# Optimization experiments

Hardware: AMD Instinct MI355X
Metric: run time of the kernel (lower is better)

The kernel has to match this reference:

```python
import jax, jax.numpy as jnp
import numpy as np

NUM_CLASSES = 81
OUTPUT_SIZE = 19
NMS_THRESH = 0.45
TOP_K = 400          # pre-NMS candidates per class == max_output_size of tf NMS
KEEP_TOP_K = 200
CONF_THRESH = 0.01
MASK_CONF_THRESH = 0.6
B = 8
P = 24564


def setup_inputs() -> dict:
    key = jax.random.key(0)
    k1, k2, k3, k4 = jax.random.split(key, 4)
    # structured x = [loc | conf | priorbox | variances] so the decode math is realistic
    loc = 0.1 * jax.random.normal(k1, (B, P, 4), dtype=jnp.float32)
    conf = jax.random.uniform(k2, (B, P, NUM_CLASSES), dtype=jnp.float32)
    cxcy = jax.random.uniform(k3, (P, 2), minval=0.05, maxval=0.95)
    wh = jax.random.uniform(k4, (P, 2), minval=0.05, maxval=0.3)
    pmin = jnp.clip(cxcy - 0.5 * wh, 0.0, 1.0)
    pmax = jnp.clip(cxcy + 0.5 * wh, 0.0, 1.0)
    priors = jnp.broadcast_to(jnp.concatenate([pmin, pmax], -1), (B, P, 4)).astype(jnp.float32)
    variances = jnp.full((B, P, 4), 0.1, dtype=jnp.float32)
    x = jnp.concatenate([loc, conf, priors, variances], -1)
    return {"x": x}


def decode_boxes(loc, prior, var):
    pw = prior[..., 2] - prior[..., 0]
    ph = prior[..., 3] - prior[..., 1]
    pcx = 0.5 * (prior[..., 2] + prior[..., 0])
    pcy = 0.5 * (prior[..., 3] + prior[..., 1])
    cx = loc[..., 0] * pw * var[..., 0] + pcx
    cy = loc[..., 1] * pw * var[..., 1] + pcy  # uses prior_width, faithful to original code
    w = jnp.exp(loc[..., 2] * var[..., 2]) * pw
    h = jnp.exp(loc[..., 3] * var[..., 3]) * ph
    box = jnp.stack([cx - 0.5 * w, cy - 0.5 * h, cx + 0.5 * w, cy + 0.5 * h], -1)
    return jnp.clip(box, 0.0, 1.0)


def iou_matrix(b):  # [N,4] xyxy -> [N,N]
    area = (b[:, 2] - b[:, 0]) * (b[:, 3] - b[:, 1])
    ix1 = jnp.maximum(b[:, None, 0], b[None, :, 0])
    iy1 = jnp.maximum(b[:, None, 1], b[None, :, 1])
    ix2 = jnp.minimum(b[:, None, 2], b[None, :, 2])
    iy2 = jnp.minimum(b[:, None, 3], b[None, :, 3])
    inter = jnp.maximum(ix2 - ix1, 0.0) * jnp.maximum(iy2 - iy1, 0.0)
    union = area[:, None] + area[None, :] - inter
    return jnp.where(union > 0.0, inter / union, 0.0)


def greedy_nms(iou, valid):  # candidates already sorted desc by score
    n = valid.shape[0]
    def body(kept, i):
        sup = jnp.any(kept & (iou[i] > NMS_THRESH))
        return kept.at[i].set(valid[i] & ~sup), None
    kept, _ = jax.lax.scan(body, jnp.zeros(n, dtype=bool), jnp.arange(n))
    return kept


def _forward(x):
    b = x.shape[0]
    loc = x[..., :4]
    conf = x[..., 4:4 + NUM_CLASSES]
    prior = x[..., -8:-4]
    var = x[..., -4:]
    boxes = decode_boxes(loc, prior, var)                        # [B,P,4]
    cls_conf = jnp.swapaxes(conf[..., 1:], 1, 2)                 # [B,C-1,P] (skip background class 0)
    masked = jnp.where(cls_conf > CONF_THRESH, cls_conf, -1.0)
    scores, idx = jax.lax.top_k(masked, TOP_K)                   # [B,C-1,K]
    cand = jnp.take_along_axis(boxes[:, None], idx[..., None], axis=2)  # [B,C-1,K,4]
    valid = scores > CONF_THRESH
    iou = jax.vmap(jax.vmap(iou_matrix))(cand)                   # [B,C-1,K,K]
    kept = jax.vmap(jax.vmap(greedy_nms))(iou, valid)            # [B,C-1,K]
    labels = jnp.broadcast_to(jnp.arange(1, NUM_CLASSES)[None, :, None], scores.shape)
    det_scores = jnp.where(kept, scores, -1.0).reshape(b, -1)
    det_boxes = cand.reshape(b, -1, 4)
    det_labels = labels.reshape(b, -1)
    order = jnp.argsort(-det_scores, axis=1)[:, :KEEP_TOP_K]     # sort desc by conf, keep_top_k=200
    top_s = jnp.take_along_axis(det_scores, order, 1)            # [B,200]
    top_b = jnp.take_along_axis(det_boxes, order[..., None], 1)  # [B,200,4]
    top_l = jnp.take_along_axis(det_labels, order, 1)            # [B,200]

    def rasterize(s, bx, lb):
        vld = s >= MASK_CONF_THRESH
        co = jnp.round(bx * OUTPUT_SIZE).astype(jnp.int32)       # [K,4] x1,y1,x2,y2
        g = jnp.arange(OUTPUT_SIZE)
        cover = ((g[None, :, None] >= co[:, 1, None, None]) & (g[None, :, None] < co[:, 3, None, None]) &
                 (g[None, None, :] >= co[:, 0, None, None]) & (g[None, None, :] < co[:, 2, None, None]) &
                 vld[:, None, None])                             # [K,S,S]
        chan = lb - 1                                            # label-1 channel, as in original
        kidx = jnp.arange(KEEP_TOP_K)
        def per_channel(c):
            cov = cover & (chan == c)[:, None, None]
            win = jnp.max(jnp.where(cov, kidx[:, None, None], -1), axis=0)  # [S,S]
            return jnp.where(win >= 0, s[jnp.clip(win, 0)], 0.0)
        return jnp.transpose(jax.vmap(per_channel)(jnp.arange(NUM_CLASSES)), (1, 2, 0))

    return jax.vmap(rasterize)(top_s, top_b, top_l)              # [B,S,S,C]


def reference(x):
    return _forward(x)
```

## Files before the change

kernel.cpp:

```cpp
#include <hip/hip_runtime.h>

#define NB 8
#define NP 24564
#define NCLS 80
#define TOPK 400
#define KEEPK 200
#define OUTS 19
#define NCELL (OUTS * OUTS)
#define DETN (NCLS * TOPK)
#define CKS 32008
#define ROWS 64
#define CHUNKS ((NP + ROWS - 1) / ROWS)
#define CAP 1024
#define T0 0.972f
#define NT 512
#define LCAP 16
#define CSTR 16
#define WTASK 2704
#define SKW(i) ((unsigned)(i) + ((unsigned)(i) >> 5))
#define SELN (TOPK + (TOPK >> 5) + 4)

__device__ __forceinline__ unsigned f2ord(float f) {
    unsigned u = __float_as_uint(f);
    return (u & 0x80000000u) ? ~u : (u | 0x80000000u);
}
__device__ __forceinline__ float ord2f(unsigned k) {
    unsigned u = (k & 0x80000000u) ? (k & 0x7fffffffu) : ~k;
    return __uint_as_float(u);
}
__device__ __forceinline__ unsigned bin16(unsigned key) {
    int b = (int)(key >> 16) - 0xBC00;
    b = b < 0 ? 0 : (b > 1023 ? 1023 : b);
    return (unsigned)b;
}

__device__ __forceinline__ unsigned long long shfl_xor_u64(unsigned long long v, int mask) {
    unsigned lo = (unsigned)__shfl_xor((int)(unsigned)v, mask);
    unsigned hi = (unsigned)__shfl_xor((int)(v >> 32), mask);
    return ((unsigned long long)hi << 32) | lo;
}

__device__ __forceinline__ void regsort1024(unsigned long long& a0, unsigned long long& a1,
                                            unsigned long long* sc, unsigned t) {
    const unsigned e0 = 2u * t;
#pragma unroll
    for (unsigned k = 2; k <= 1024; k <<= 1) {
#pragma unroll
        for (unsigned j = k >> 1; j >= 128; j >>= 1) {
            sc[e0] = a0; sc[e0 + 1] = a1;
            __syncthreads();
            unsigned p0 = e0 ^ j;
            unsigned long long b0 = sc[p0], b1 = sc[p0 + 1];
            bool km = ((e0 & k) == 0u) ^ ((e0 & j) != 0u);
            a0 = km ? (a0 > b0 ? a0 : b0) : (a0 < b0 ? a0 : b0);
            a1 = km ? (a1 > b1 ? a1 : b1) : (a1 < b1 ? a1 : b1);
            __syncthreads();
        }
#pragma unroll
        for (unsigned j = ((k >> 1) < 64u ? (k >> 1) : 64u); j >= 2; j >>= 1) {
            unsigned long long b0 = shfl_xor_u64(a0, (int)(j >> 1));
            unsigned long long b1 = shfl_xor_u64(a1, (int)(j >> 1));
            bool km = ((e0 & k) == 0u) ^ ((e0 & j) != 0u);
            a0 = km ? (a0 > b0 ? a0 : b0) : (a0 < b0 ? a0 : b0);
            a1 = km ? (a1 > b1 ? a1 : b1) : (a1 < b1 ? a1 : b1);
        }
        {
            bool dir = ((e0 & k) == 0u);
            unsigned long long mx = a0 > a1 ? a0 : a1;
            unsigned long long mn = a0 > a1 ? a1 : a0;
            a0 = dir ? mx : mn;
            a1 = dir ? mn : mx;
        }
    }
}

__device__ __forceinline__ void bitonic_desc(unsigned long long* cand, unsigned S, int tid) {
    for (unsigned k = 2; k <= S; k <<= 1)
        for (unsigned j = k >> 1; j; j >>= 1) {
            for (unsigned i = tid; i < S; i += NT) {
                unsigned l = i ^ j;
                if (l > i) {
                    unsigned long long a = cand[i], bq = cand[l];
                    bool sw = ((i & k) == 0) ? (a < bq) : (a > bq);
                    if (sw) { cand[i] = bq; cand[l] = a; }
                }
            }
            __syncthreads();
        }
}

__global__ __launch_bounds__(256) void kZ(unsigned* __restrict__ ccnt,
                                          unsigned* __restrict__ gflag,
                                          unsigned* __restrict__ kcnt) {
    int t = blockIdx.x * 256 + threadIdx.x;
    for (int i = t; i < NB * NCLS * CSTR; i += gridDim.x * 256) ccnt[i] = 0u;
    if (t < NB * NCLS) gflag[t] = 0u;
    if (t < NB * 16) kcnt[t] = 0u;
}

__global__ __launch_bounds__(NT) void kA(const float* __restrict__ x,
                                         float4* __restrict__ boxes,
                                         unsigned long long* __restrict__ pcand,
                                         unsigned* __restrict__ ccnt,
                                         unsigned* __restrict__ gflag) {
    __shared__ float tile[ROWS * 93];
    __shared__ unsigned long long list[NCLS * LCAP];
    __shared__ unsigned lcnt[NCLS];
    __shared__ unsigned lbase[NCLS];

    int blk = blockIdx.x;
    int b = blk / CHUNKS, chunk = blk % CHUNKS;
    int p0 = chunk * ROWS;
    int nrows = NP - p0; if (nrows > ROWS) nrows = ROWS;
    const float* src = x + (size_t)(b * NP + p0) * 93;
    int total4 = (nrows * 93) >> 2;
    const float4* s4 = (const float4*)src;
    float4* t4 = (float4*)tile;
    for (int e = threadIdx.x; e < total4; e += NT) t4[e] = s4[e];
    __syncthreads();

    int row = threadIdx.x & 63;
    int lane = row;
    int cg = threadIdx.x >> 6;
    unsigned p = (unsigned)(p0 + row);
    bool rowOk = row < nrows;
    for (int c = cg; c < NCLS; c += (NT / 64)) {
        float v = rowOk ? tile[row * 93 + 5 + c] : -1.0f;
        bool pred = v > T0;
        unsigned long long bal = __ballot(pred);
        if (pred) {
            unsigned rank = (unsigned)__popcll(bal & ((1ull << lane) - 1ull));
            if (rank < LCAP)
                list[c * LCAP + rank] =
                    ((unsigned long long)f2ord(v) << 32) | (unsigned)(~p);
        }
        if (lane == 0) lcnt[c] = (unsigned)__popcll(bal);
    }

    if (threadIdx.x < nrows) {
        const float* r = tile + threadIdx.x * 93;
        float l0 = r[0], l1 = r[1], l2 = r[2], l3 = r[3];
        float px1 = r[85], py1 = r[86], px2 = r[87], py2 = r[88];
        float v0 = r[89], v1 = r[90], v2 = r[91], v3 = r[92];
        float pw = px2 - px1, ph = py2 - py1;
        float pcx = 0.5f * (px2 + px1), pcy = 0.5f * (py2 + py1);
        float cx = l0 * pw * v0 + pcx;
        float cy = l1 * pw * v1 + pcy;
        float w = expf(l2 * v2) * pw;
        float h = expf(l3 * v3) * ph;
        float x1 = fminf(fmaxf(cx - 0.5f * w, 0.f), 1.f);
        float y1 = fminf(fmaxf(cy - 0.5f * h, 0.f), 1.f);
        float x2 = fminf(fmaxf(cx + 0.5f * w, 0.f), 1.f);
        float y2 = fminf(fmaxf(cy + 0.5f * h, 0.f), 1.f);
        boxes[(size_t)b * NP + p0 + threadIdx.x] = make_float4(x1, y1, x2, y2);
    }
    __syncthreads();

    if (threadIdx.x < NCLS) {
        unsigned n = lcnt[threadIdx.x];
        unsigned wr = (n > LCAP) ? LCAP : n;
        lbase[threadIdx.x] =
            wr ? atomicAdd(&ccnt[(b * NCLS + threadIdx.x) * CSTR], wr) : 0u;
        lcnt[threadIdx.x] = wr;
        if (n > LCAP) gflag[b * NCLS + threadIdx.x] = 1u;
    }
    __syncthreads();

    for (int idx = threadIdx.x; idx < NCLS * LCAP; idx += NT) {
        int c = idx >> 4, i = idx & (LCAP - 1);
        if ((unsigned)i < lcnt[c]) {
            unsigned pos = lbase[c] + (unsigned)i;
            if (pos < CAP)
                pcand[((size_t)(b * NCLS + c) << 10) + pos] = list[idx];
        }
    }
}

__device__ void select_strided(const float* __restrict__ src, unsigned needed,
                               unsigned long long* cand,
                               unsigned* hist, unsigned* aux, unsigned* scal,
                               int tid) {
    for (int i = tid; i < 1024; i += NT) hist[i] = 0u;
    if (tid == 0) { scal[0] = 0u; scal[1] = 0u; scal[2] = 0u; scal[3] = 0u; }
    __syncthreads();
    for (int p = tid; p < NP; p += NT) {
        float v = src[(size_t)p * 93];
        float m = (v > 0.01f) ? v : -1.0f;
        atomicAdd(&hist[bin16(f2ord(m))], 1u);
    }
    __syncthreads();
    unsigned h0 = 0, h1 = 0, h2 = 0, h3 = 0;
    if (tid < 256) {
        h0 = hist[4 * tid]; h1 = hist[4 * tid + 1];
        h2 = hist[4 * tid + 2]; h3 = hist[4 * tid + 3];
        aux[tid] = h0 + h1 + h2 + h3;
    }
    __syncthreads();
    for (int d = 1; d < 256; d <<= 1) {
        unsigned v = 0u;
        if (tid < 256 && tid + d < 256) v = aux[tid + d];
        __syncthreads();
        if (tid < 256) aux[tid] += v;
        __syncthreads();
    }
    if (tid < 256) {
        unsigned above = (tid < 255) ? aux[tid + 1] : 0u;
        unsigned s3 = above + h3, s2 = s3 + h2, s1 = s2 + h1, s0 = s1 + h0;
        if (s0 >= needed && s1 < needed) { scal[0] = 4 * tid;     scal[1] = s1;    scal[2] = s0; }
        if (s1 >= needed && s2 < needed) { scal[0] = 4 * tid + 1; scal[1] = s2;    scal[2] = s1; }
        if (s2 >= needed && s3 < needed) { scal[0] = 4 * tid + 2; scal[1] = s3;    scal[2] = s2; }
        if (s3 >= needed && above < needed) { scal[0] = 4 * tid + 3; scal[1] = above; scal[2] = s3; }
    }
    __syncthreads();
    unsigned cb = scal[0], countHigh = scal[1], countAt = scal[2];
    unsigned cut8 = 0;
    if (countAt > CAP) {
        if (tid < 256) aux[tid] = 0u;
        __syncthreads();
        for (int p = tid; p < NP; p += NT) {
            float v = src[(size_t)p * 93];
            float m = (v > 0.01f) ? v : -1.0f;
            unsigned k = f2ord(m);
            if (bin16(k) == cb) atomicAdd(&aux[(k >> 8) & 255u], 1u);
        }
        __syncthreads();
        for (int d = 1; d < 256; d <<= 1) {
            unsigned v = 0u;
            if (tid < 256 && tid + d < 256) v = aux[tid + d];
            __syncthreads();
            if (tid < 256) aux[tid] += v;
            __syncthreads();
        }
        if (tid < 256) {
            unsigned suf8 = aux[tid];
            unsigned sufN = (tid < 255) ? aux[tid + 1] : 0u;
            unsigned need2 = needed - countHigh;
            if (suf8 >= need2 && sufN < need2) scal[3] = (unsigned)tid;
        }
        __syncthreads();
        cut8 = scal[3];
    }
    __syncthreads();
    if (tid == 0) scal[1] = 0u;
    __syncthreads();
    for (int p = tid; p < NP; p += NT) {
        float v = src[(size_t)p * 93];
        float m = (v > 0.01f) ? v : -1.0f;
        unsigned key = f2ord(m);
        unsigned b16 = bin16(key);
        bool take = (b16 > cb) || (b16 == cb && ((key >> 8) & 255u) >= cut8);
        if (take) {
            unsigned pos = atomicAdd(&scal[1], 1u);
            if (pos < CAP) cand[pos] = ((unsigned long long)key << 32) | (unsigned)(~p);
        }
    }
    __syncthreads();
    unsigned cc = scal[1]; if (cc > CAP) cc = CAP;
    for (unsigned i = tid; i < CAP; i += NT) if (i >= cc) cand[i] = 0ull;
    __syncthreads();
    bitonic_desc(cand, (cc <= 512u) ? 512u : (unsigned)CAP, tid);
}

union ScratchU {
    unsigned long long sc[1024];
    unsigned iouRowP[WTASK];
    struct { unsigned long long cand[CAP]; unsigned hist[1024]; unsigned aux[256]; } fb;
};

__global__ __launch_bounds__(NT) void kNms(const float* __restrict__ x,
                                           const float4* __restrict__ boxes,
                                           const unsigned long long* __restrict__ pcand,
                                           const unsigned* __restrict__ ccnt,
                                           const unsigned* __restrict__ gflag,
                                           unsigned long long* __restrict__ ckeys,
                                           float4* __restrict__ cboxes,
                                           unsigned* __restrict__ kcnt) {
    __shared__ ScratchU U;
    __shared__ float4 selBox[SELN];
    __shared__ float selArea[SELN];
    __shared__ unsigned selKey[SELN];
    __shared__ unsigned scal[4];
    __shared__ unsigned keptWords[13];

    int b = blockIdx.x / NCLS, c = blockIdx.x % NCLS;
    int tid = threadIdx.x;
    unsigned t = (unsigned)tid;

    unsigned count = ccnt[(b * NCLS + c) * CSTR];
    bool fast = (gflag[b * NCLS + c] == 0u) && (count >= TOPK) && (count <= CAP);
    unsigned long long a0, a1;
    if (fast) {
        const ulonglong2* src2 =
            (const ulonglong2*)(pcand + ((size_t)(b * NCLS + c) << 10));
        ulonglong2 vv = src2[t];
        a0 = (2u * t     < count) ? vv.x : 0ull;
        a1 = (2u * t + 1 < count) ? vv.y : 0ull;
        regsort1024(a0, a1, U.sc, t);
    } else {
        select_strided(x + (size_t)b * NP * 93 + 5 + c, TOPK,
                       U.fb.cand, U.fb.hist, U.fb.aux, scal, tid);
        a0 = U.fb.cand[2u * t];
        a1 = U.fb.cand[2u * t + 1];
    }
    if (t < TOPK / 2) {
        unsigned i0 = ~(unsigned)a0; if (i0 >= NP) i0 = 0;
        unsigned i1 = ~(unsigned)a1; if (i1 >= NP) i1 = 0;
        float4 b0 = boxes[(size_t)b * NP + i0];
        float4 b1 = boxes[(size_t)b * NP + i1];
        selBox[SKW(2u * t)] = b0;            selBox[SKW(2u * t + 1)] = b1;
        selArea[SKW(2u * t)] = (b0.z - b0.x) * (b0.w - b0.y);
        selArea[SKW(2u * t + 1)] = (b1.z - b1.x) * (b1.w - b1.y);
        selKey[SKW(2u * t)] = (unsigned)(a0 >> 32);
        selKey[SKW(2u * t + 1)] = (unsigned)(a1 >> 32);
    }
    __syncthreads();

    for (int T = tid; T < WTASK; T += NT) {
        int b0i = (int)(sqrtf((float)T * 0.0625f + 0.25f) - 0.5f);
        while (16 * (b0i + 1) * (b0i + 2) <= T) ++b0i;
        while (b0i > 0 && 16 * b0i * (b0i + 1) > T) --b0i;
        int off = T - 16 * b0i * (b0i + 1);
        int rr = off / (b0i + 1);
        int w = off - rr * (b0i + 1);
        int r = 32 * b0i + rr;
        float4 br = selBox[SKW(r)];
        float ar = selArea[SKW(r)];
        unsigned word = 0;
#pragma unroll 8
        for (int jj = 0; jj < 32; ++jj) {
            int j = w * 32 + jj;
            float4 bj = selBox[SKW(j)];
            float ix = fminf(br.z, bj.z) - fmaxf(br.x, bj.x);
            float iy = fminf(br.w, bj.w) - fmaxf(br.y, bj.y);
            float inter = fmaxf(ix, 0.f) * fmaxf(iy, 0.f);
            float uni = ar + selArea[SKW(j)] - inter;
            word |= (unsigned)(inter > 0.45f * uni) << jj;
        }
        U.iouRowP[T] = word;
    }
    __syncthreads();

    if (tid < 64) {
        unsigned lane = t;
        unsigned myKept = 0;
        const unsigned VALID_KEY = f2ord(0.01f);
        unsigned ro = 0;
        unsigned w = (lane < 1u) ? U.iouRowP[lane] : 0u;
        unsigned keyCur = selKey[SKW(0)];
        for (int i = 0; i < TOPK; ++i) {
            unsigned nwi = (unsigned)(i >> 5) + 1u;
            unsigned ron = ro + nwi;
            unsigned wn = 0u, keyNext = 0u;
            if (i < TOPK - 1) {
                if (lane <= (unsigned)((i + 1) >> 5)) wn = U.iouRowP[ron + lane];
                keyNext = selKey[SKW(i + 1)];
            }
            bool hit = (w & myKept) != 0u;
            unsigned long long bal = __ballot(hit);
            bool kept = (keyCur > VALID_KEY) && (bal == 0ull);
            if (kept && lane == (unsigned)(i >> 5)) myKept |= 1u << (i & 31);
            w = wn; keyCur = keyNext; ro = ron;
        }
        if (lane < 13) keptWords[lane] = myKept;
    }
    __syncthreads();

    if (tid == 0) {
        unsigned total = 0;
        for (int w = 0; w < 13; ++w) total += __popc(keptWords[w]);
        scal[2] = atomicAdd(&kcnt[b * 16], total);
    }
    __syncthreads();
    unsigned base = scal[2];
    size_t kb = (size_t)b * CKS;
    size_t bb = (size_t)b * DETN;
    for (int k = tid; k < TOPK; k += NT) {
        unsigned flat = (unsigned)(c * TOPK + k);
        cboxes[bb + flat] = selBox[SKW(k)];
        bool kept = (keptWords[k >> 5] >> (k & 31)) & 1u;
        if (kept) {
            unsigned rank = 0;
            int wi = k >> 5;
            for (int w = 0; w < wi; ++w) rank += __popc(keptWords[w]);
            rank += __popc(keptWords[wi] & ((1u << (k & 31)) - 1u));
            ckeys[kb + base + rank] =
                ((unsigned long long)selKey[SKW(k)] << 32) | (unsigned)(~flat);
        }
    }
}

struct HistU { unsigned hist[1024]; unsigned aux[256]; };

__global__ __launch_bounds__(NT) void kC(const unsigned long long* __restrict__ ckeys,
                                         const float4* __restrict__ cboxes,
                                         const unsigned* __restrict__ kcnt,
                                         float* __restrict__ out) {
    __shared__ unsigned long long cand[CAP];
    __shared__ unsigned long long scK[CAP];
    __shared__ HistU S;
    __shared__ unsigned scal[4];
    __shared__ float eS[KEEPK];
    __shared__ int eC0[KEEPK], eC1[KEEPK], eC2[KEEPK], eC3[KEEPK];
    __shared__ int eCh[KEEPK];

    int b = blockIdx.x;
    int tid = threadIdx.x;
    unsigned t = (unsigned)tid;
    const ulonglong2* k2 = (const ulonglong2*)(ckeys + (size_t)b * CKS);
    int n = (int)kcnt[b * 16]; if (n > DETN) n = DETN;
    int n2 = (n + 1) >> 1;
    const unsigned needed = KEEPK;

    for (int i = tid; i < 1024; i += NT) S.hist[i] = 0u;
    if (tid == 0) { scal[0] = 0u; scal[1] = 0u; scal[2] = 0u; scal[3] = 0u; }
    __syncthreads();
    for (int i = tid; i < n2; i += NT) {
        ulonglong2 v = k2[i];
        atomicAdd(&S.hist[bin16((unsigned)(v.x >> 32))], 1u);
        if (2 * i + 1 < n) atomicAdd(&S.hist[bin16((unsigned)(v.y >> 32))], 1u);
    }
    __syncthreads();
    unsigned h0 = 0, h1 = 0, h2 = 0, h3 = 0;
    if (tid < 256) {
        h0 = S.hist[4 * tid]; h1 = S.hist[4 * tid + 1];
        h2 = S.hist[4 * tid + 2]; h3 = S.hist[4 * tid + 3];
        S.aux[tid] = h0 + h1 + h2 + h3;
    }
    __syncthreads();
    for (int d = 1; d < 256; d <<= 1) {
        unsigned v = 0u;
        if (tid < 256 && tid + d < 256) v = S.aux[tid + d];
        __syncthreads();
        if (tid < 256) S.aux[tid] += v;
        __syncthreads();
    }
    if (tid < 256) {
        unsigned above = (tid < 255) ? S.aux[tid + 1] : 0u;
        unsigned s3 = above + h3, s2 = s3 + h2, s1 = s2 + h1, s0 = s1 + h0;
        if (s0 >= needed && s1 < needed) { scal[0] = 4 * tid;     scal[1] = s1;    scal[2] = s0; }
        if (s1 >= needed && s2 < needed) { scal[0] = 4 * tid + 1; scal[1] = s2;    scal[2] = s1; }
        if (s2 >= needed && s3 < needed) { scal[0] = 4 * tid + 2; scal[1] = s3;    scal[2] = s2; }
        if (s3 >= needed && above < needed) { scal[0] = 4 * tid + 3; scal[1] = above; scal[2] = s3; }
    }
    __syncthreads();
    unsigned cb = scal[0], countHigh = scal[1], countAt = scal[2];
    unsigned cut8 = 0;
    if (countAt > CAP) {
        if (tid < 256) S.aux[tid] = 0u;
        __syncthreads();
        for (int i = tid; i < n2; i += NT) {
            ulonglong2 v = k2[i];
            unsigned kx = (unsigned)(v.x >> 32), ky = (unsigned)(v.y >> 32);
            if (bin16(kx) == cb) atomicAdd(&S.aux[(kx >> 8) & 255u], 1u);
            if (2 * i + 1 < n && bin16(ky) == cb) atomicAdd(&S.aux[(ky >> 8) & 255u], 1u);
        }
        __syncthreads();
        for (int d = 1; d < 256; d <<= 1) {
            unsigned v = 0u;
            if (tid < 256 && tid + d < 256) v = S.aux[tid + d];
            __syncthreads();
            if (tid < 256) S.aux[tid] += v;
            __syncthreads();
        }
        if (tid < 256) {
            unsigned suf8 = S.aux[tid];
            unsigned sufN = (tid < 255) ? S.aux[tid + 1] : 0u;
            unsigned need2 = needed - countHigh;
            if (suf8 >= need2 && sufN < need2) scal[3] = (unsigned)tid;
        }
        __syncthreads();
        cut8 = scal[3];
    }
    __syncthreads();
    if (tid == 0) scal[1] = 0u;
    __syncthreads();
    for (int i = tid; i < n2; i += NT) {
        ulonglong2 v = k2[i];
#pragma unroll
        for (int c = 0; c < 2; ++c) {
            if (c && 2 * i + 1 >= n) continue;
            unsigned long long key = c ? v.y : v.x;
            unsigned kh = (unsigned)(key >> 32);
            unsigned b16 = bin16(kh);
            bool take = (b16 > cb) || (b16 == cb && ((kh >> 8) & 255u) >= cut8);
            if (take) {
                unsigned pos = atomicAdd(&scal[1], 1u);
                if (pos < CAP) cand[pos] = key;
            }
        }
    }
    __syncthreads();
    unsigned cc = scal[1]; if (cc > CAP) cc = CAP;
    for (unsigned i = tid; i < CAP; i += NT) if (i >= cc) cand[i] = 0ull;
    __syncthreads();
    unsigned long long a0 = cand[2u * t], a1 = cand[2u * t + 1];
    __syncthreads();
    regsort1024(a0, a1, scK, t);

    if (t < KEEPK / 2) {
#pragma unroll
        for (int q = 0; q < 2; ++q) {
            unsigned long long K = q ? a1 : a0;
            unsigned k = 2u * t + q;
            unsigned key = (unsigned)(K >> 32);
            unsigned flat = ~(unsigned)K;
            if (flat >= DETN) flat = 0;
            float4 bx = cboxes[(size_t)b * DETN + flat];
            eS[k] = (key == 0u) ? -1.0f : ord2f(key);
            eC0[k] = (int)rintf(bx.x * (float)OUTS);
            eC1[k] = (int)rintf(bx.y * (float)OUTS);
            eC2[k] = (int)rintf(bx.z * (float)OUTS);
            eC3[k] = (int)rintf(bx.w * (float)OUTS);
            eCh[k] = (int)(flat / TOPK);
        }
    }
    __syncthreads();

    for (int cell = tid; cell < NCELL; cell += NT) {
        int y = cell / OUTS, x = cell % OUTS;
        float* o = out + ((size_t)b * NCELL + cell) * 81;
        for (int ch = 0; ch < 81; ++ch) o[ch] = 0.f;
        for (int k = 0; k < KEEPK; ++k) {
            float s = eS[k];
            if (s < 0.6f) continue;
            if (y >= eC1[k] && y < eC3[k] && x >= eC0[k] && x < eC2[k])
                o[eCh[k]] = s;
        }
    }
}

extern "C" void kernel_launch(void* const* d_in, const int* in_sizes, int n_in,
                              void* d_out, int out_size, void* d_ws, size_t ws_size,
                              hipStream_t stream) {
    const float* x = (const float*)d_in[0];
    float* out = (float*)d_out;

    float4* boxes   = (float4*)d_ws;
    float4* cboxes  = boxes + (size_t)NB * NP;
    unsigned long long* ckeys = (unsigned long long*)(cboxes + (size_t)NB * DETN);
    unsigned long long* pcand = ckeys + (size_t)NB * CKS;
    unsigned* ccnt = (unsigned*)(pcand + ((size_t)NB * NCLS << 10));
    unsigned* gflag = ccnt + NB * NCLS * CSTR;
    unsigned* kcnt  = gflag + NB * NCLS;

    kZ<<<40, 256, 0, stream>>>(ccnt, gflag, kcnt);
    kA<<<NB * CHUNKS, NT, 0, stream>>>(x, boxes, pcand, ccnt, gflag);
    kNms<<<NB * NCLS, NT, 0, stream>>>(x, boxes, pcand, ccnt, gflag, ckeys, cboxes, kcnt);
    kC<<<NB, NT, 0, stream>>>(ckeys, cboxes, kcnt, out);
}
```

Before: 261.3 us.

## Register-tile IoU bitmask over four rows and deepen NMS scan prefetch

The IoU bitmask build now has each thread compute four rows against one 32-column word, using a precomputed shared task table instead of sqrt-based triangular index decoding. This reuses each column box load four times. The serial greedy scan prefetches eight rows ahead in registers and replaces the per-row key test with a count of valid candidates computed by ballot. These changes cut LDS traffic and index math at the cost of more registers, and they rely on valid candidates forming a prefix of the sorted order.

```diff
diff --git a/kernel.cpp b/kernel.cpp
--- a/kernel.cpp
+++ b/kernel.cpp
@@ -17,6 +17,7 @@
 #define LCAP 16
 #define CSTR 16
 #define WTASK 2704
+#define TILN 676
 #define SKW(i) ((unsigned)(i) + ((unsigned)(i) >> 5))
 #define SELN (TOPK + (TOPK >> 5) + 4)
 
@@ -279,12 +280,22 @@
     __shared__ float4 selBox[SELN];
     __shared__ float selArea[SELN];
     __shared__ unsigned selKey[SELN];
+    __shared__ unsigned short taskGW[TILN];
     __shared__ unsigned scal[4];
+    __shared__ unsigned Vsh;
     __shared__ unsigned keptWords[13];
 
     int b = blockIdx.x / NCLS, c = blockIdx.x % NCLS;
     int tid = threadIdx.x;
     unsigned t = (unsigned)tid;
+
+    if (tid == 0) Vsh = 0u;
+    if (tid < 100) {
+        unsigned g = t, v = g >> 3, r = g & 7u;
+        unsigned O = g + 4u * v * (v - 1u) + r * v;
+        for (unsigned w = 0; w <= v; ++w)
+            taskGW[O + w] = (unsigned short)((g << 4) | w);
+    }
 
     unsigned count = ccnt[(b * NCLS + c) * CSTR];
     bool fast = (gflag[b * NCLS + c] == 0u) && (count >= TOPK) && (count <= CAP);
@@ -302,6 +313,7 @@
         a0 = U.fb.cand[2u * t];
         a1 = U.fb.cand[2u * t + 1];
     }
+    const unsigned VALID_KEY = f2ord(0.01f);
     if (t < TOPK / 2) {
         unsigned i0 = ~(unsigned)a0; if (i0 >= NP) i0 = 0;
         unsigned i1 = ~(unsigned)a1; if (i1 >= NP) i1 = 0;
@@ -313,54 +325,72 @@
         selKey[SKW(2u * t)] = (unsigned)(a0 >> 32);
         selKey[SKW(2u * t + 1)] = (unsigned)(a1 >> 32);
     }
-    __syncthreads();
-
-    for (int T = tid; T < WTASK; T += NT) {
-        int b0i = (int)(sqrtf((float)T * 0.0625f + 0.25f) - 0.5f);
-        while (16 * (b0i + 1) * (b0i + 2) <= T) ++b0i;
-        while (b0i > 0 && 16 * b0i * (b0i + 1) > T) --b0i;
-        int off = T - 16 * b0i * (b0i + 1);
-        int rr = off / (b0i + 1);
-        int w = off - rr * (b0i + 1);
-        int r = 32 * b0i + rr;
-        float4 br = selBox[SKW(r)];
-        float ar = selArea[SKW(r)];
-        unsigned word = 0;
+    {
+        bool v0 = (t < TOPK / 2) && ((unsigned)(a0 >> 32) > VALID_KEY);
+        bool v1 = (t < TOPK / 2) && ((unsigned)(a1 >> 32) > VALID_KEY);
+        unsigned long long bv0 = __ballot(v0), bv1 = __ballot(v1);
+        if ((t & 63u) == 0u)
+            atomicAdd(&Vsh, (unsigned)(__popcll(bv0) + __popcll(bv1)));
+    }
+    __syncthreads();
+
+    for (int T = tid; T < TILN; T += NT) {
+        unsigned gw = (unsigned)taskGW[T];
+        unsigned g = gw >> 4, w = gw & 15u;
+        unsigned r0 = 4u * g;
+        float4 br0 = selBox[SKW(r0)];     float ar0 = selArea[SKW(r0)];
+        float4 br1 = selBox[SKW(r0 + 1)]; float ar1 = selArea[SKW(r0 + 1)];
+        float4 br2 = selBox[SKW(r0 + 2)]; float ar2 = selArea[SKW(r0 + 2)];
+        float4 br3 = selBox[SKW(r0 + 3)]; float ar3 = selArea[SKW(r0 + 3)];
+        unsigned w0 = 0, w1 = 0, w2 = 0, w3 = 0;
 #pragma unroll 8
         for (int jj = 0; jj < 32; ++jj) {
-            int j = w * 32 + jj;
+            int j = (int)(w * 32u) + jj;
             float4 bj = selBox[SKW(j)];
-            float ix = fminf(br.z, bj.z) - fmaxf(br.x, bj.x);
-            float iy = fminf(br.w, bj.w) - fmaxf(br.y, bj.y);
-            float inter = fmaxf(ix, 0.f) * fmaxf(iy, 0.f);
-            float uni = ar + selArea[SKW(j)] - inter;
-            word |= (unsigned)(inter > 0.45f * uni) << jj;
-        }
-        U.iouRowP[T] = word;
+            float aj = selArea[SKW(j)];
+#define IOU1(BR, AR, WRD) { \
+            float ix = fminf(BR.z, bj.z) - fmaxf(BR.x, bj.x); \
+            float iy = fminf(BR.w, bj.w) - fmaxf(BR.y, bj.y); \
+            float inter = fmaxf(ix, 0.f) * fmaxf(iy, 0.f); \
+            float uni = AR + aj - inter; \
+            WRD |= (unsigned)(inter > 0.45f * uni) << jj; }
+            IOU1(br0, ar0, w0) IOU1(br1, ar1, w1)
+            IOU1(br2, ar2, w2) IOU1(br3, ar3, w3)
+#undef IOU1
+        }
+        unsigned band = g >> 3;
+        unsigned baseo = (band + 1u) * (16u * band + (r0 & 31u)) + w;
+        U.iouRowP[baseo]                   = w0;
+        U.iouRowP[baseo +      (band + 1u)] = w1;
+        U.iouRowP[baseo + 2u * (band + 1u)] = w2;
+        U.iouRowP[baseo + 3u * (band + 1u)] = w3;
     }
     __syncthreads();
 
     if (tid < 64) {
         unsigned lane = t;
         unsigned myKept = 0;
-        const unsigned VALID_KEY = f2ord(0.01f);
-        unsigned ro = 0;
-        unsigned w = (lane < 1u) ? U.iouRowP[lane] : 0u;
-        unsigned keyCur = selKey[SKW(0)];
-        for (int i = 0; i < TOPK; ++i) {
-            unsigned nwi = (unsigned)(i >> 5) + 1u;
-            unsigned ron = ro + nwi;
-            unsigned wn = 0u, keyNext = 0u;
-            if (i < TOPK - 1) {
-                if (lane <= (unsigned)((i + 1) >> 5)) wn = U.iouRowP[ron + lane];
-                keyNext = selKey[SKW(i + 1)];
-            }
-            bool hit = (w & myKept) != 0u;
-            unsigned long long bal = __ballot(hit);
-            bool kept = (keyCur > VALID_KEY) && (bal == 0ull);
-            if (kept && lane == (unsigned)(i >> 5)) myKept |= 1u << (i & 31);
-            w = wn; keyCur = keyNext; ro = ron;
-        }
+        unsigned V = Vsh;
+        unsigned q0 = U.iouRowP[0 + lane], q1 = U.iouRowP[1 + lane];
+        unsigned q2 = U.iouRowP[2 + lane], q3 = U.iouRowP[3 + lane];
+        unsigned q4 = U.iouRowP[4 + lane], q5 = U.iouRowP[5 + lane];
+        unsigned q6 = U.iouRowP[6 + lane], q7 = U.iouRowP[7 + lane];
+#define STEP(Q, II) { \
+        unsigned w_ = Q; \
+        int ip_ = (II) + 8; \
+        if (ip_ < TOPK) { \
+            unsigned bb_ = (unsigned)ip_ >> 5; \
+            Q = U.iouRowP[(bb_ + 1u) * (16u * bb_ + ((unsigned)ip_ & 31u)) + lane]; \
+        } \
+        bool hit_ = (w_ & myKept) != 0u; \
+        unsigned long long bal_ = __ballot(hit_); \
+        if ((unsigned)(II) < V && bal_ == 0ull && lane == ((unsigned)(II) >> 5)) \
+            myKept |= 1u << ((II) & 31); }
+        for (int i = 0; i < TOPK; i += 8) {
+            STEP(q0, i)     STEP(q1, i + 1) STEP(q2, i + 2) STEP(q3, i + 3)
+            STEP(q4, i + 4) STEP(q5, i + 5) STEP(q6, i + 6) STEP(q7, i + 7)
+        }
+#undef STEP
         if (lane < 13) keptWords[lane] = myKept;
     }
     __syncthreads();
```

Result: faster. 241.8 us (-7.4%).
